# Performance work log

Hardware: AMD Instinct MI355X
Metric: run time of the kernel (lower is better)

Reference implementation:

```python
import jax, jax.numpy as jnp
import numpy as np

NUM_HEADS = 12
LOCAL_WINDOW = 7


def setup_inputs() -> dict:
    key = jax.random.key(0)
    k1, k2, k3 = jax.random.split(key, 3)
    B, N, C = 2, 2048, 768
    x = jax.random.normal(k1, (B, N, C), dtype=jnp.float32)
    w_qkv = jax.random.normal(k2, (3 * C, C), dtype=jnp.float32) * (C ** -0.5)
    w_proj = jax.random.normal(k3, (C, C), dtype=jnp.float32) * (C ** -0.5)
    b_proj = jnp.zeros((C,), dtype=jnp.float32)
    return {"x": x, "w_qkv": w_qkv, "w_proj": w_proj, "b_proj": b_proj}


def reference(x, w_qkv, w_proj, b_proj):
    B, N, C = x.shape
    H = NUM_HEADS
    Dh = C // H
    scale = Dh ** -0.5
    # local-window additive mask: 0 within |i-j|<=w, -inf outside (vectorized)
    idx = jnp.arange(N)
    local_mask = jnp.where(
        jnp.abs(idx[:, None] - idx[None, :]) <= LOCAL_WINDOW, 0.0, -jnp.inf
    ).astype(x.dtype)
    qkv = x @ w_qkv.T
    qkv = qkv.reshape(B, N, 3, H, Dh).transpose(2, 0, 3, 1, 4)
    q, k, v = qkv[0], qkv[1], qkv[2]
    attn = jnp.einsum("bhnd,bhmd->bhnm", q, k) * scale
    attn = attn + local_mask[None, None, :, :]
    attn = jax.nn.softmax(attn, axis=-1)
    out = jnp.einsum("bhnm,bhmd->bhnd", attn, v)
    out = out.transpose(0, 2, 1, 3).reshape(B, N, C)
    return out @ w_proj.T + b_proj
```

## Files before the change

### kernel.cpp

```cpp
#include <hip/hip_runtime.h>
#include <hip/hip_bf16.h>

typedef __bf16 bf16;
typedef bf16 bf16x4 __attribute__((ext_vector_type(4)));
typedef bf16 bf16x8 __attribute__((ext_vector_type(8)));
typedef float floatx4 __attribute__((ext_vector_type(4)));

#define GLOBAL_AS __attribute__((address_space(1)))
#define LDS_AS __attribute__((address_space(3)))

__device__ __forceinline__ void hard_barrier() {
    asm volatile("" ::: "memory");
    __builtin_amdgcn_s_barrier();
    asm volatile("" ::: "memory");
}

__global__ __launch_bounds__(256)
void cvt3_f32_bf16(const float* __restrict__ s0, const float* __restrict__ s1,
                   const float* __restrict__ s2, bf16* __restrict__ d0,
                   bf16* __restrict__ d1, bf16* __restrict__ d2,
                   int n0, int n1, int n2)
{
    int t = blockIdx.x * blockDim.x + threadIdx.x;
    const float* s; bf16* d; int i;
    if (t < n0)                { s = s0; d = d0; i = t; }
    else if (t < n0 + n1)      { s = s1; d = d1; i = t - n0; }
    else if (t < n0 + n1 + n2) { s = s2; d = d2; i = t - n0 - n1; }
    else return;
    float4 v = ((const float4*)s)[i];
    bf16x4 o = { (bf16)v.x, (bf16)v.y, (bf16)v.z, (bf16)v.w };
    ((bf16x4*)d)[i] = o;
}

template<typename CT, int M, int N, int K, int LDA, int LDC>
__global__ __launch_bounds__(512, 2)
void gemm8p_bt(const bf16* __restrict__ A, const bf16* __restrict__ W,
               CT* __restrict__ C)
{
    constexpr int NT = K / 64;
    __shared__ __align__(16) bf16 lds[2][2][256 * 64];

    const int tid  = threadIdx.x;
    const int lane = tid & 63;
    const int wave = tid >> 6;

    int lin = blockIdx.x;
    const int chx = gridDim.x >> 3;
    lin = (lin & 7) * chx + (lin >> 3);
    const int bx = lin / (N / 256);
    const int by = lin % (N / 256);
    const int row0 = bx * 256;
    const int col0 = by * 256;

    const int wm = (wave & 1) * 128;
    const int wn = (wave >> 1) * 64;

    const int fr  = lane & 15;
    const int fks = lane >> 4;
    const int fr7 = fr & 7;

    const int rl = tid >> 3;
    const int sl = tid & 7;
    const int ss = sl ^ (rl & 7);

    floatx4 acc[8][4] = {};

    auto stage = [&](const bf16* G, int ldg, int g0, int k0, bf16* Ld) {
        #pragma unroll
        for (int c = 0; c < 4; ++c) {
            const bf16* src = G + (size_t)(g0 + c * 64 + rl) * ldg + k0 + ss * 8;
            __builtin_amdgcn_global_load_lds((const GLOBAL_AS void*)src,
                (LDS_AS void*)(Ld + c * 4096 + wave * 512), 16, 0, 0);
        }
    };

    bf16x8 afA[4][2], bf0[2][2], bf1[2][2];

    auto loadA = [&](const bf16* Ab, int qi) {
        #pragma unroll
        for (int ii = 0; ii < 4; ++ii)
            #pragma unroll
            for (int kk = 0; kk < 2; ++kk)
                afA[ii][kk] = *(const bf16x8*)(Ab
                    + (wm + (qi + ii) * 16 + fr) * 64
                    + (((kk * 4 + fks) ^ fr7) * 8));
    };
    auto loadB = [&](const bf16* Bb, int qj, bf16x8 (&bb)[2][2]) {
        #pragma unroll
        for (int jj = 0; jj < 2; ++jj)
            #pragma unroll
            for (int kk = 0; kk < 2; ++kk)
                bb[jj][kk] = *(const bf16x8*)(Bb
                    + (wn + (qj + jj) * 16 + fr) * 64
                    + (((kk * 4 + fks) ^ fr7) * 8));
    };
    auto mfmaQ = [&](int qi, int qj, bf16x8 (&bb)[2][2]) {
        __builtin_amdgcn_s_setprio(1);
        #pragma unroll
        for (int ii = 0; ii < 4; ++ii)
            #pragma unroll
            for (int jj = 0; jj < 2; ++jj)
                #pragma unroll
                for (int kk = 0; kk < 2; ++kk)
                    acc[qi + ii][qj + jj] =
                        __builtin_amdgcn_mfma_f32_16x16x32_bf16(
                            afA[ii][kk], bb[jj][kk], acc[qi + ii][qj + jj],
                            0, 0, 0);
        __builtin_amdgcn_s_setprio(0);
        hard_barrier();
    };

    stage(A, LDA, row0, 0, lds[0][0]);
    stage(W, K,   col0, 0, lds[0][1]);

    for (int t = 0; t < NT; ++t) {
        const int buf = t & 1;
        const bf16* Ab = lds[buf][0];
        const bf16* Bb = lds[buf][1];
        if (t + 1 < NT) {
            stage(A, LDA, row0, (t + 1) * 64, lds[buf ^ 1][0]);
            stage(W, K,   col0, (t + 1) * 64, lds[buf ^ 1][1]);
            asm volatile("s_waitcnt vmcnt(8)" ::: "memory");
        } else {
            asm volatile("s_waitcnt vmcnt(0)" ::: "memory");
        }
        hard_barrier();

        loadA(Ab, 0);
        loadB(Bb, 0, bf0);
        loadB(Bb, 2, bf1);
        mfmaQ(0, 0, bf0);
        mfmaQ(0, 2, bf1);
        loadA(Ab, 4);
        mfmaQ(4, 2, bf1);
        mfmaQ(4, 0, bf0);
    }

    const int fc  = lane & 15;
    const int fr4 = (lane >> 4) * 4;
    #pragma unroll
    for (int i = 0; i < 8; ++i)
        #pragma unroll
        for (int j = 0; j < 4; ++j) {
            const int col = col0 + wn + j * 16 + fc;
            #pragma unroll
            for (int r = 0; r < 4; ++r) {
                const int row = row0 + wm + i * 16 + fr4 + r;
                C[(size_t)row * LDC + col] = (CT)acc[i][j][r];
            }
        }
}

template<typename CT, bool AF32, bool WF32, int TM, int M, int N, int K,
         int LDA, int LDC>
__global__ __launch_bounds__(256, 2)
void gemm_bt(const void* __restrict__ Av, const void* __restrict__ Wv,
             CT* __restrict__ C, const float* __restrict__ bias)
{
    constexpr int MI = TM / 32;
    __shared__ __align__(16) bf16 As[TM * 32];
    __shared__ __align__(16) bf16 Bs[128 * 32];

    const int tid  = threadIdx.x;
    const int lane = tid & 63;
    const int wave = tid >> 6;

    const int lin = blockIdx.y * gridDim.x + blockIdx.x;
    const int ch  = gridDim.x >> 3;
    const int xcd = lin & 7;
    const int rr  = lin >> 3;
    const int bx  = xcd * ch + (rr % ch);
    const int by  = rr / ch;

    const int row0 = bx * TM;
    const int col0 = by * 128;

    const int wm = (wave & 1) * (TM / 2);
    const int wn = (wave >> 1) * 64;

    floatx4 acc[MI][4] = {};

    const int fr = lane & 15;
    const int fk = (lane >> 4) * 8;

    const int lr = lane >> 2;
    const int lk = (lane & 3) * 8;

    for (int k0 = 0; k0 < K; k0 += 32) {
        if (AF32) {
            constexpr int NV = TM * 4;
            #pragma unroll
            for (int c = 0; c < NV / 256; ++c) {
                const int idx = tid + c * 256;
                const int r   = idx >> 2;
                const int cb  = (idx & 3) * 8;
                const float4* g = (const float4*)((const float*)Av
                                   + (size_t)(row0 + r) * LDA + k0 + cb);
                float4 g0 = g[0], g1 = g[1];
                bf16x8 va;
                va[0]=(bf16)g0.x; va[1]=(bf16)g0.y; va[2]=(bf16)g0.z; va[3]=(bf16)g0.w;
                va[4]=(bf16)g1.x; va[5]=(bf16)g1.y; va[6]=(bf16)g1.z; va[7]=(bf16)g1.w;
                *(bf16x8*)(As + r * 32 + cb) = va;
            }
        } else {
            constexpr int CAW = TM / 64;
            #pragma unroll
            for (int c = 0; c < CAW; ++c) {
                const int chunk = wave * CAW + c;
                const int r = chunk * 16 + lr;
                const bf16* gA = (const bf16*)Av + (size_t)(row0 + r) * LDA + k0 + lk;
                __builtin_amdgcn_global_load_lds((const GLOBAL_AS void*)gA,
                                                 (LDS_AS void*)(As + chunk * 512),
                                                 16, 0, 0);
            }
        }
        if (WF32) {
            #pragma unroll
            for (int c = 0; c < 2; ++c) {
                const int idx = tid + c * 256;
                const int r   = idx >> 2;
                const int cb  = (idx & 3) * 8;
                const float4* g = (const float4*)((const float*)Wv
                                   + (size_t)(col0 + r) * K + k0 + cb);
                float4 g0 = g[0], g1 = g[1];
                bf16x8 vw;
                vw[0]=(bf16)g0.x; vw[1]=(bf16)g0.y; vw[2]=(bf16)g0.z; vw[3]=(bf16)g0.w;
                vw[4]=(bf16)g1.x; vw[5]=(bf16)g1.y; vw[6]=(bf16)g1.z; vw[7]=(bf16)g1.w;
                *(bf16x8*)(Bs + r * 32 + cb) = vw;
            }
        } else {
            #pragma unroll
            for (int c = 0; c < 2; ++c) {
                const int chunk = wave * 2 + c;
                const int r = chunk * 16 + lr;
                const bf16* gB = (const bf16*)Wv + (size_t)(col0 + r) * K + k0 + lk;
                __builtin_amdgcn_global_load_lds((const GLOBAL_AS void*)gB,
                                                 (LDS_AS void*)(Bs + chunk * 512),
                                                 16, 0, 0);
            }
        }
        __syncthreads();

        bf16x8 af[MI], bfr[4];
        #pragma unroll
        for (int i = 0; i < MI; ++i)
            af[i]  = *(const bf16x8*)(As + (wm + i * 16 + fr) * 32 + fk);
        #pragma unroll
        for (int j = 0; j < 4; ++j)
            bfr[j] = *(const bf16x8*)(Bs + (wn + j * 16 + fr) * 32 + fk);
        #pragma unroll
        for (int i = 0; i < MI; ++i)
            #pragma unroll
            for (int j = 0; j < 4; ++j)
                acc[i][j] = __builtin_amdgcn_mfma_f32_16x16x32_bf16(
                    af[i], bfr[j], acc[i][j], 0, 0, 0);

        __syncthreads();
    }

    const int fc  = lane & 15;
    const int fr4 = (lane >> 4) * 4;
    #pragma unroll
    for (int i = 0; i < MI; ++i) {
        #pragma unroll
        for (int j = 0; j < 4; ++j) {
            const int col = col0 + wn + j * 16 + fc;
            const float b = bias ? bias[col] : 0.0f;
            #pragma unroll
            for (int r = 0; r < 4; ++r) {
                const int row = row0 + wm + i * 16 + fr4 + r;
                C[(size_t)row * LDC + col] = (CT)(acc[i][j][r] + b);
            }
        }
    }
}

__global__ __launch_bounds__(256)
void attn_tile(const bf16* __restrict__ qkv, bf16* __restrict__ aout)
{
    __shared__ __align__(16) bf16 Vt[4][64][40];
    __shared__ __align__(16) bf16 Ps[4][16][40];

    const int w    = threadIdx.x >> 6;
    const int lane = threadIdx.x & 63;
    const int c    = lane & 15;
    const int q    = lane >> 4;
    int bid = blockIdx.x;
    bid = (bid & 7) * 96 + (bid >> 3);
    const int wid  = bid * 4 + w;
    const int it   = wid & 127;
    const int bh   = wid >> 7;
    const int h    = bh % 12;
    const int b    = bh / 12;
    const int I0   = it * 16;
    const int bbase = b * 2048;
    const int j0   = I0 - 7;

    #pragma unroll
    for (int itr = 0; itr < 4; ++itr) {
        int idx = itr * 64 + lane;
        int row = idx >> 3;
        int dc  = (idx & 7) * 8;
        int jc  = j0 + row; jc = jc < 0 ? 0 : (jc > 2047 ? 2047 : jc);
        const bf16* base = qkv + (size_t)(bbase + jc) * 2304 + 1536 + h * 64 + dc;
        bf16x8 vv = *(const bf16x8*)base;
        #pragma unroll
        for (int e = 0; e < 8; ++e) {
            int d    = dc + e;
            int col2 = (row * 2) ^ (((d >> 3) & 3) << 4);
            *(bf16*)((char*)&Vt[w][d][0] + col2) = vv[e];
        }
    }

    const bf16* qrow = qkv + (size_t)(bbase + I0 + c) * 2304 + h * 64;
    bf16x8 aq0 = *(const bf16x8*)(qrow + q * 8);
    bf16x8 aq1 = *(const bf16x8*)(qrow + 32 + q * 8);

    floatx4 st[2] = {};
    #pragma unroll
    for (int t = 0; t < 2; ++t) {
        int jr = j0 + t * 16 + c;
        jr = jr < 0 ? 0 : (jr > 2047 ? 2047 : jr);
        const bf16* krow = qkv + (size_t)(bbase + jr) * 2304 + 768 + h * 64;
        bf16x8 k0 = *(const bf16x8*)(krow + q * 8);
        bf16x8 k1 = *(const bf16x8*)(krow + 32 + q * 8);
        st[t] = __builtin_amdgcn_mfma_f32_16x16x32_bf16(aq0, k0, st[t], 0, 0, 0);
        st[t] = __builtin_amdgcn_mfma_f32_16x16x32_bf16(aq1, k1, st[t], 0, 0, 0);
    }

    float s[2][4];
    #pragma unroll
    for (int t = 0; t < 2; ++t)
        #pragma unroll
        for (int r = 0; r < 4; ++r) {
            int il = q * 4 + r;
            int jl = t * 16 + c;
            int ja = j0 + jl;
            bool valid = (jl >= il) && (jl <= il + 14) && (ja >= 0) && (ja < 2048);
            s[t][r] = valid ? st[t][r] * 0.125f : -1e30f;
        }

    float l[4], p[2][4];
    #pragma unroll
    for (int r = 0; r < 4; ++r) {
        float m2 = fmaxf(s[0][r], s[1][r]);
        #pragma unroll
        for (int mk = 1; mk < 16; mk <<= 1) m2 = fmaxf(m2, __shfl_xor(m2, mk, 64));
        p[0][r] = __expf(s[0][r] - m2);
        p[1][r] = __expf(s[1][r] - m2);
        float l2 = p[0][r] + p[1][r];
        #pragma unroll
        for (int mk = 1; mk < 16; mk <<= 1) l2 += __shfl_xor(l2, mk, 64);
        l[r] = l2;
    }

    #pragma unroll
    for (int r = 0; r < 4; ++r) {
        Ps[w][q * 4 + r][c]      = (bf16)p[0][r];
        Ps[w][q * 4 + r][16 + c] = (bf16)p[1][r];
    }

    bf16x8 ap = *(const bf16x8*)(&Ps[w][c][q * 8]);
    floatx4 ov[4];
    #pragma unroll
    for (int nt = 0; nt < 4; ++nt) {
        int dr = nt * 16 + c;
        int cb = (q * 16) ^ (((dr >> 3) & 3) << 4);
        bf16x8 vf = *(const bf16x8*)((const char*)&Vt[w][dr][0] + cb);
        floatx4 z = {};
        ov[nt] = __builtin_amdgcn_mfma_f32_16x16x32_bf16(ap, vf, z, 0, 0, 0);
    }

    float rl[4];
    #pragma unroll
    for (int r = 0; r < 4; ++r) rl[r] = 1.0f / l[r];
    #pragma unroll
    for (int r = 0; r < 4; ++r) {
        bf16* orow = aout + (size_t)(bbase + I0 + q * 4 + r) * 768 + h * 64;
        #pragma unroll
        for (int nt = 0; nt < 4; ++nt)
            orow[nt * 16 + c] = (bf16)(ov[nt][r] * rl[r]);
    }
}

extern "C" void kernel_launch(void* const* d_in, const int* in_sizes, int n_in,
                              void* d_out, int out_size, void* d_ws, size_t ws_size,
                              hipStream_t stream)
{
    const float* x      = (const float*)d_in[0];
    const float* w_qkv  = (const float*)d_in[1];
    const float* w_proj = (const float*)d_in[2];
    const float* b_proj = (const float*)d_in[3];
    float* out = (float*)d_out;

    bf16* qkv = (bf16*)d_ws;
    const size_t QKV_B  = (size_t)4096 * 2304 * 2;
    const size_t AO_B   = (size_t)4096 * 768 * 2;
    const size_t XB_B   = (size_t)4096 * 768 * 2;
    const size_t WQKV_B = (size_t)2304 * 768 * 2;
    const size_t WPRJ_B = (size_t)768 * 768 * 2;

    if (ws_size >= QKV_B + AO_B + XB_B + WQKV_B + WPRJ_B) {
        bf16* aout = (bf16*)((char*)d_ws + QKV_B);
        bf16* xb   = (bf16*)((char*)aout + AO_B);
        bf16* wqb  = (bf16*)((char*)xb + XB_B);
        bf16* wpb  = (bf16*)((char*)wqb + WQKV_B);

        const int n0 = 4096 * 768 / 4, n1 = 2304 * 768 / 4, n2 = 768 * 768 / 4;
        cvt3_f32_bf16<<<dim3((n0 + n1 + n2) / 256), 256, 0, stream>>>(
            x, w_qkv, w_proj, xb, wqb, wpb, n0, n1, n2);

        gemm8p_bt<bf16, 4096, 2304, 768, 768, 2304>
            <<<dim3(144), 512, 0, stream>>>(xb, wqb, qkv);

        attn_tile<<<dim3(768), 256, 0, stream>>>(qkv, aout);

        gemm_bt<float, false, false, 64, 4096, 768, 768, 768, 768>
            <<<dim3(64, 6), 256, 0, stream>>>(aout, wpb, out, b_proj);
    } else {
        gemm_bt<bf16, true, true, 128, 4096, 2304, 768, 768, 2304>
            <<<dim3(32, 18), 256, 0, stream>>>(x, w_qkv, qkv, nullptr);

        bf16* aout = (bf16*)((char*)d_ws + QKV_B);
        attn_tile<<<dim3(768), 256, 0, stream>>>(qkv, aout);

        gemm_bt<float, false, true, 64, 4096, 768, 768, 768, 768>
            <<<dim3(64, 6), 256, 0, stream>>>(aout, w_proj, out, b_proj);
    }
}
```

Before: 123.5 us.

## Retile QKV GEMM to 256x192 tiles and add double-buffered projection GEMM

```diff
diff --git a/kernel.cpp b/kernel.cpp
--- a/kernel.cpp
+++ b/kernel.cpp
@@ -38,7 +38,7 @@
                CT* __restrict__ C)
 {
     constexpr int NT = K / 64;
-    __shared__ __align__(16) bf16 lds[2][2][256 * 64];
+    __shared__ __align__(16) bf16 lds[2][(256 + 192) * 64];
 
     const int tid  = threadIdx.x;
     const int lane = tid & 63;
@@ -47,13 +47,13 @@
     int lin = blockIdx.x;
     const int chx = gridDim.x >> 3;
     lin = (lin & 7) * chx + (lin >> 3);
-    const int bx = lin / (N / 256);
-    const int by = lin % (N / 256);
+    const int bx = lin / (N / 192);
+    const int by = lin % (N / 192);
     const int row0 = bx * 256;
-    const int col0 = by * 256;
+    const int col0 = by * 192;
 
     const int wm = (wave & 1) * 128;
-    const int wn = (wave >> 1) * 64;
+    const int wn = (wave >> 1) * 48;
 
     const int fr  = lane & 15;
     const int fks = lane >> 4;
@@ -63,18 +63,26 @@
     const int sl = tid & 7;
     const int ss = sl ^ (rl & 7);
 
-    floatx4 acc[8][4] = {};
-
-    auto stage = [&](const bf16* G, int ldg, int g0, int k0, bf16* Ld) {
+    floatx4 acc[8][3] = {};
+
+    auto stageA = [&](int k0, bf16* Ld) {
         #pragma unroll
         for (int c = 0; c < 4; ++c) {
-            const bf16* src = G + (size_t)(g0 + c * 64 + rl) * ldg + k0 + ss * 8;
+            const bf16* src = A + (size_t)(row0 + c * 64 + rl) * LDA + k0 + ss * 8;
             __builtin_amdgcn_global_load_lds((const GLOBAL_AS void*)src,
                 (LDS_AS void*)(Ld + c * 4096 + wave * 512), 16, 0, 0);
         }
     };
-
-    bf16x8 afA[4][2], bf0[2][2], bf1[2][2];
+    auto stageB = [&](int k0, bf16* Ld) {
+        #pragma unroll
+        for (int c = 0; c < 3; ++c) {
+            const bf16* src = W + (size_t)(col0 + c * 64 + rl) * K + k0 + ss * 8;
+            __builtin_amdgcn_global_load_lds((const GLOBAL_AS void*)src,
+                (LDS_AS void*)(Ld + c * 4096 + wave * 512), 16, 0, 0);
+        }
+    };
+
+    bf16x8 afA[4][2], b01[2][2], b2[1][2];
 
     auto loadA = [&](const bf16* Ab, int qi) {
         #pragma unroll
@@ -85,16 +93,23 @@
                     + (wm + (qi + ii) * 16 + fr) * 64
                     + (((kk * 4 + fks) ^ fr7) * 8));
     };
-    auto loadB = [&](const bf16* Bb, int qj, bf16x8 (&bb)[2][2]) {
+    auto loadB01 = [&](const bf16* Bb) {
         #pragma unroll
         for (int jj = 0; jj < 2; ++jj)
             #pragma unroll
             for (int kk = 0; kk < 2; ++kk)
-                bb[jj][kk] = *(const bf16x8*)(Bb
-                    + (wn + (qj + jj) * 16 + fr) * 64
+                b01[jj][kk] = *(const bf16x8*)(Bb
+                    + (wn + jj * 16 + fr) * 64
                     + (((kk * 4 + fks) ^ fr7) * 8));
     };
-    auto mfmaQ = [&](int qi, int qj, bf16x8 (&bb)[2][2]) {
+    auto loadB2 = [&](const bf16* Bb) {
+        #pragma unroll
+        for (int kk = 0; kk < 2; ++kk)
+            b2[0][kk] = *(const bf16x8*)(Bb
+                + (wn + 2 * 16 + fr) * 64
+                + (((kk * 4 + fks) ^ fr7) * 8));
+    };
+    auto mfma16 = [&](int qi) {
         __builtin_amdgcn_s_setprio(1);
         #pragma unroll
         for (int ii = 0; ii < 4; ++ii)
@@ -102,38 +117,48 @@
             for (int jj = 0; jj < 2; ++jj)
                 #pragma unroll
                 for (int kk = 0; kk < 2; ++kk)
-                    acc[qi + ii][qj + jj] =
-                        __builtin_amdgcn_mfma_f32_16x16x32_bf16(
-                            afA[ii][kk], bb[jj][kk], acc[qi + ii][qj + jj],
-                            0, 0, 0);
+                    acc[qi + ii][jj] = __builtin_amdgcn_mfma_f32_16x16x32_bf16(
+                        afA[ii][kk], b01[jj][kk], acc[qi + ii][jj], 0, 0, 0);
         __builtin_amdgcn_s_setprio(0);
         hard_barrier();
     };
-
-    stage(A, LDA, row0, 0, lds[0][0]);
-    stage(W, K,   col0, 0, lds[0][1]);
+    auto mfma8 = [&](int qi) {
+        __builtin_amdgcn_s_setprio(1);
+        #pragma unroll
+        for (int ii = 0; ii < 4; ++ii)
+            #pragma unroll
+            for (int kk = 0; kk < 2; ++kk)
+                acc[qi + ii][2] = __builtin_amdgcn_mfma_f32_16x16x32_bf16(
+                    afA[ii][kk], b2[0][kk], acc[qi + ii][2], 0, 0, 0);
+        __builtin_amdgcn_s_setprio(0);
+        hard_barrier();
+    };
+
+    stageA(0, lds[0]);
+    stageB(0, lds[0] + 256 * 64);
 
     for (int t = 0; t < NT; ++t) {
         const int buf = t & 1;
-        const bf16* Ab = lds[buf][0];
-        const bf16* Bb = lds[buf][1];
+        const bf16* Ab = lds[buf];
+        const bf16* Bb = lds[buf] + 256 * 64;
+        asm volatile("s_waitcnt lgkmcnt(0)" ::: "memory");
         if (t + 1 < NT) {
-            stage(A, LDA, row0, (t + 1) * 64, lds[buf ^ 1][0]);
-            stage(W, K,   col0, (t + 1) * 64, lds[buf ^ 1][1]);
-            asm volatile("s_waitcnt vmcnt(8)" ::: "memory");
+            stageA((t + 1) * 64, lds[buf ^ 1]);
+            stageB((t + 1) * 64, lds[buf ^ 1] + 256 * 64);
+            asm volatile("s_waitcnt vmcnt(7)" ::: "memory");
         } else {
             asm volatile("s_waitcnt vmcnt(0)" ::: "memory");
         }
         hard_barrier();
 
         loadA(Ab, 0);
-        loadB(Bb, 0, bf0);
-        loadB(Bb, 2, bf1);
-        mfmaQ(0, 0, bf0);
-        mfmaQ(0, 2, bf1);
+        loadB01(Bb);
+        loadB2(Bb);
+        mfma16(0);
+        mfma8(0);
         loadA(Ab, 4);
-        mfmaQ(4, 2, bf1);
-        mfmaQ(4, 0, bf0);
+        mfma8(4);
+        mfma16(4);
     }
 
     const int fc  = lane & 15;
@@ -141,7 +166,7 @@
     #pragma unroll
     for (int i = 0; i < 8; ++i)
         #pragma unroll
-        for (int j = 0; j < 4; ++j) {
+        for (int j = 0; j < 3; ++j) {
             const int col = col0 + wn + j * 16 + fc;
             #pragma unroll
             for (int r = 0; r < 4; ++r) {
@@ -149,6 +174,110 @@
                 C[(size_t)row * LDC + col] = (CT)acc[i][j][r];
             }
         }
+}
+
+template<typename CT, int TM, int M, int N, int K, int LDA, int LDC>
+__global__ __launch_bounds__(256, 2)
+void gemm_bt_p(const bf16* __restrict__ A, const bf16* __restrict__ W,
+               CT* __restrict__ C, const float* __restrict__ bias)
+{
+    constexpr int MI  = TM / 32;
+    constexpr int CAW = TM / 64;
+    constexpr int NT  = K / 32;
+    __shared__ __align__(16) bf16 As[2][TM * 32];
+    __shared__ __align__(16) bf16 Bs[2][128 * 32];
+
+    const int tid  = threadIdx.x;
+    const int lane = tid & 63;
+    const int wave = tid >> 6;
+
+    const int lin = blockIdx.y * gridDim.x + blockIdx.x;
+    const int ch  = gridDim.x >> 3;
+    const int xcd = lin & 7;
+    const int rr  = lin >> 3;
+    const int bx  = xcd * ch + (rr % ch);
+    const int by  = rr / ch;
+
+    const int row0 = bx * TM;
+    const int col0 = by * 128;
+
+    const int wm = (wave & 1) * (TM / 2);
+    const int wn = (wave >> 1) * 64;
+
+    floatx4 acc[MI][4] = {};
+
+    const int fr = lane & 15;
+    const int fk = (lane >> 4) * 8;
+
+    const int lr = lane >> 2;
+    const int lk = (lane & 3) * 8;
+
+    auto stage = [&](int k0, int buf) {
+        #pragma unroll
+        for (int c = 0; c < CAW; ++c) {
+            const int chunk = wave * CAW + c;
+            const int r = chunk * 16 + lr;
+            const bf16* gA = A + (size_t)(row0 + r) * LDA + k0 + lk;
+            __builtin_amdgcn_global_load_lds((const GLOBAL_AS void*)gA,
+                                             (LDS_AS void*)(As[buf] + chunk * 512),
+                                             16, 0, 0);
+        }
+        #pragma unroll
+        for (int c = 0; c < 2; ++c) {
+            const int chunk = wave * 2 + c;
+            const int r = chunk * 16 + lr;
+            const bf16* gB = W + (size_t)(col0 + r) * K + k0 + lk;
+            __builtin_amdgcn_global_load_lds((const GLOBAL_AS void*)gB,
+                                             (LDS_AS void*)(Bs[buf] + chunk * 512),
+                                             16, 0, 0);
+        }
+    };
+
+    stage(0, 0);
+    for (int t = 0; t < NT; ++t) {
+        const int buf = t & 1;
+        if (t + 1 < NT) {
+            stage((t + 1) * 32, buf ^ 1);
+            if (TM == 64) asm volatile("s_waitcnt vmcnt(3)" ::: "memory");
+            else          asm volatile("s_waitcnt vmcnt(4)" ::: "memory");
+        } else {
+            asm volatile("s_waitcnt vmcnt(0)" ::: "memory");
+        }
+        hard_barrier();
+
+        bf16x8 af[MI], bfr[4];
+        #pragma unroll
+        for (int i = 0; i < MI; ++i)
+            af[i]  = *(const bf16x8*)(As[buf] + (wm + i * 16 + fr) * 32 + fk);
+        #pragma unroll
+        for (int j = 0; j < 4; ++j)
+            bfr[j] = *(const bf16x8*)(Bs[buf] + (wn + j * 16 + fr) * 32 + fk);
+        #pragma unroll
+        for (int i = 0; i < MI; ++i)
+            #pragma unroll
+            for (int j = 0; j < 4; ++j)
+                acc[i][j] = __builtin_amdgcn_mfma_f32_16x16x32_bf16(
+                    af[i], bfr[j], acc[i][j], 0, 0, 0);
+
+        asm volatile("s_waitcnt lgkmcnt(0)" ::: "memory");
+        hard_barrier();
+    }
+
+    const int fc  = lane & 15;
+    const int fr4 = (lane >> 4) * 4;
+    #pragma unroll
+    for (int i = 0; i < MI; ++i) {
+        #pragma unroll
+        for (int j = 0; j < 4; ++j) {
+            const int col = col0 + wn + j * 16 + fc;
+            const float b = bias ? bias[col] : 0.0f;
+            #pragma unroll
+            for (int r = 0; r < 4; ++r) {
+                const int row = row0 + wm + i * 16 + fr4 + r;
+                C[(size_t)row * LDC + col] = (CT)(acc[i][j][r] + b);
+            }
+        }
+    }
 }
 
 template<typename CT, bool AF32, bool WF32, int TM, int M, int N, int K,
@@ -411,11 +540,11 @@
             x, w_qkv, w_proj, xb, wqb, wpb, n0, n1, n2);
 
         gemm8p_bt<bf16, 4096, 2304, 768, 768, 2304>
-            <<<dim3(144), 512, 0, stream>>>(xb, wqb, qkv);
+            <<<dim3(192), 512, 0, stream>>>(xb, wqb, qkv);
 
         attn_tile<<<dim3(768), 256, 0, stream>>>(qkv, aout);
 
-        gemm_bt<float, false, false, 64, 4096, 768, 768, 768, 768>
+        gemm_bt_p<float, 64, 4096, 768, 768, 768, 768>
             <<<dim3(64, 6), 256, 0, stream>>>(aout, wpb, out, b_proj);
     } else {
         gemm_bt<bf16, true, true, 128, 4096, 2304, 768, 768, 2304>
```

Measured after the change: 118.7 us. 3.9% less time.
